# Performance work log

Hardware: AMD Instinct MI355X
Metric: run time of the kernel (lower is better)

The kernel has to match this reference:

```python
import jax, jax.numpy as jnp
import numpy as np

# irreps '64x0e+32x1o+16x2e' as (mul, ir_dim, is_scalar)
IRREPS = [(64, 1, True), (32, 3, False), (16, 5, False)]
DIM = sum(m * d for m, d, _ in IRREPS)          # 240
NUM_FEATURES = sum(m for m, _, _ in IRREPS)      # 112
NUM_SCALAR = sum(m for m, _, s in IRREPS if s)   # 64
NUM_TYPE = 10
EPS = 1e-5
BATCH = 200000


def setup_inputs() -> dict:
    key = jax.random.key(0)
    k1, k2 = jax.random.split(key)
    x = jax.random.normal(k1, (BATCH, DIM), dtype=jnp.float32)
    input_type = jax.random.randint(k2, (BATCH,), 0, NUM_TYPE)
    weight = jnp.ones((NUM_TYPE, NUM_FEATURES), dtype=jnp.float32)
    bias = jnp.zeros((NUM_TYPE, NUM_SCALAR), dtype=jnp.float32)
    return {"x": x, "input_type": input_type, "weight": weight, "bias": bias}


def _type_mean(vals, input_type, counts):
    # scatter_mean over the batch dim into NUM_TYPE slots
    s = jax.ops.segment_sum(vals, input_type, num_segments=NUM_TYPE)
    return s / counts[:, None]


def reference(x, input_type, weight, bias):
    batch, dim = x.shape
    xr = x.reshape(batch, 1, dim)  # middle dim (no extra ... dims here)
    counts = jnp.maximum(
        jax.ops.segment_sum(jnp.ones((batch,), x.dtype), input_type, num_segments=NUM_TYPE),
        1.0,
    )
    fields = []
    ix = iw = ib = 0
    for mul, d, is_scalar in IRREPS:
        field = xr[:, :, ix:ix + mul * d].reshape(batch, -1, mul, d)
        ix += mul * d
        if is_scalar:
            fm = field.mean(1).reshape(batch, mul)                 # (batch, mul)
            fm = _type_mean(fm, input_type, counts)                # (num_type, mul)
            field = field - fm[input_type][:, None, :, None]
        # normalization='component': mean over ir dim; reduce='mean' over middle dim
        fn = jnp.square(field).mean(3).mean(1)                     # (batch, mul)
        fn = _type_mean(fn, input_type, counts)                    # (num_type, mul)
        fn = jax.lax.rsqrt(fn + EPS)
        fn = fn * weight[:, iw:iw + mul]
        iw += mul
        field = field * fn[input_type][:, None, :, None]
        if is_scalar:
            field = field + bias[:, ib:ib + mul][input_type][:, None, :, None]
            ib += mul
        fields.append(field.reshape(batch, -1, mul * d))
    out = jnp.concatenate(fields, axis=2)
    return out.reshape(batch, dim)
```

## Files before the change

### kernel.cpp

```cpp
#include <hip/hip_runtime.h>

#define DIM 240
#define NTYPE 10
#define NFEAT 112
#define NSLOT 176
#define NRED  1770
#define PSTRIDE 1792
#define RCHUNK 32
#define EPSV 1e-5f


__global__ __launch_bounds__(256) void stats_kernel(const float* __restrict__ x,
        const int* __restrict__ type, float* __restrict__ partial, int B, int nblk)
{
    const int tid = threadIdx.x;
    const bool active = tid < DIM;
    const bool isScalar = tid < 64;

    float accA[NTYPE], accB[NTYPE];
#pragma unroll
    for (int t = 0; t < NTYPE; t++) { accA[t] = 0.f; accB[t] = 0.f; }

    const float inactAdd = (tid == 255) ? 1.f : 0.f;

    auto accum = [&](int ty, float v) {
        const float v2 = v * v;
        const float addA = active ? (isScalar ? v : v2) : inactAdd;
#pragma unroll
        for (int t = 0; t < NTYPE; t++) {
            if (t == ty) { accA[t] += addA; accB[t] += v2; }
        }
    };

    const int stride = nblk * 8;
    for (int row0 = blockIdx.x * 8; row0 + 7 < B; row0 += stride) {
        int ty[8];
#pragma unroll
        for (int j = 0; j < 8; j++) ty[j] = type[row0 + j];
        float v[8];
#pragma unroll
        for (int j = 0; j < 8; j++) v[j] = 0.f;
        if (active) {
            const float* p = x + (size_t)row0 * DIM + tid;
#pragma unroll
            for (int j = 0; j < 8; j++) v[j] = p[j * DIM];
        }
#pragma unroll
        for (int j = 0; j < 8; j++) accum(ty[j], v[j]);
    }
    if (blockIdx.x == 0) {
        for (int r = B & ~7; r < B; r++) {
            const int ty0 = type[r];
            float v = active ? x[(size_t)r * DIM + tid] : 0.f;
            accum(ty0, v);
        }
    }

    __shared__ float sAcc[NRED];
    for (int i = tid; i < NRED; i += 256) sAcc[i] = 0.f;
    __syncthreads();

    if (isScalar) {
#pragma unroll
        for (int t = 0; t < NTYPE; t++) {
            sAcc[t * NSLOT + tid] = accA[t];
            sAcc[t * NSLOT + 64 + tid] = accB[t];
        }
    } else if (tid < 160) {
        const int ch = (tid - 64) / 3;
#pragma unroll
        for (int t = 0; t < NTYPE; t++)
            atomicAdd(&sAcc[t * NSLOT + 128 + ch], accA[t]);
    } else if (tid < DIM) {
        const int ch = (tid - 160) / 5;
#pragma unroll
        for (int t = 0; t < NTYPE; t++)
            atomicAdd(&sAcc[t * NSLOT + 160 + ch], accA[t]);
    } else if (tid == 255) {
#pragma unroll
        for (int t = 0; t < NTYPE; t++)
            sAcc[NTYPE * NSLOT + t] = accA[t];
    }
    __syncthreads();

    float* __restrict__ dst = partial + (size_t)blockIdx.x * PSTRIDE;
    for (int i = tid; i < NRED; i += 256) dst[i] = sAcc[i];
}

__global__ __launch_bounds__(256) void reduce1_kernel(const float* __restrict__ partial,
        float* __restrict__ gpart, int nblk)
{
    const int colChunk = blockIdx.x % 7;
    const int rowChunk = blockIdx.x / 7;
    const int col = colChunk * 256 + threadIdx.x;
    const int r0 = (rowChunk * nblk) / RCHUNK;
    const int r1 = ((rowChunk + 1) * nblk) / RCHUNK;
    float acc = 0.f;
#pragma unroll 8
    for (int r = r0; r < r1; r++)
        acc += partial[(size_t)r * PSTRIDE + col];
    gpart[rowChunk * PSTRIDE + col] = acc;
}

__global__ __launch_bounds__(256) void finalize_kernel(const float* __restrict__ gpart,
        const float* __restrict__ weight, const float* __restrict__ bias,
        float* __restrict__ params)
{
    const int t = blockIdx.x;
    const int c = threadIdx.x;

    __shared__ float scnt;
    if (c == 0) {
        float cs = 0.f;
#pragma unroll
        for (int k = 0; k < RCHUNK; k++)
            cs += gpart[k * PSTRIDE + NTYPE * NSLOT + t];
        scnt = fmaxf(cs, 1.f);
    }
    __syncthreads();
    if (c >= DIM) return;
    const float inv = 1.f / scnt;

    float sub = 0.f, mul, bia = 0.f;
    if (c < 64) {
        float S = 0.f, Q = 0.f;
#pragma unroll
        for (int k = 0; k < RCHUNK; k++) {
            const float* p = gpart + k * PSTRIDE + t * NSLOT;
            S += p[c]; Q += p[64 + c];
        }
        const float mean = S * inv;
        float var = Q * inv - mean * mean;
        var = fmaxf(var, 0.f);
        mul = rsqrtf(var + EPSV) * weight[t * NFEAT + c];
        sub = mean;
        bia = bias[t * 64 + c];
    } else if (c < 160) {
        const int ch = (c - 64) / 3;
        float N = 0.f;
#pragma unroll
        for (int k = 0; k < RCHUNK; k++)
            N += gpart[k * PSTRIDE + t * NSLOT + 128 + ch];
        mul = rsqrtf(N * inv * (1.f / 3.f) + EPSV) * weight[t * NFEAT + 64 + ch];
    } else {
        const int ch = (c - 160) / 5;
        float N = 0.f;
#pragma unroll
        for (int k = 0; k < RCHUNK; k++)
            N += gpart[k * PSTRIDE + t * NSLOT + 160 + ch];
        mul = rsqrtf(N * inv * 0.2f + EPSV) * weight[t * NFEAT + 96 + ch];
    }
    float* p = params + t * 720;
    p[c] = sub;
    p[240 + c] = mul;
    p[480 + c] = bia;
}

__global__ __launch_bounds__(256) void apply_kernel(const float* __restrict__ x,
        const int* __restrict__ type, const float* __restrict__ params,
        float* __restrict__ out, int B, int nblocks)
{
    __shared__ float4 sp[NTYPE * 180];
    const int tid = threadIdx.x;
    const float4* __restrict__ pg = (const float4*)params;
    for (int i = tid; i < NTYPE * 180; i += 256) sp[i] = pg[i];
    __syncthreads();

    const int rBase = tid / 60;
    const int c4 = tid - rBase * 60;
    const bool active = tid < 240;
    const float4* __restrict__ xv = (const float4*)x;
    float4* __restrict__ ov = (float4*)out;

    const int rstride = nblocks * 8;
    for (int row0 = blockIdx.x * 8; row0 < B; row0 += rstride) {
        const int r0 = row0 + rBase;
        const int r1 = r0 + 4;
        const bool a0 = active && r0 < B;
        const bool a1 = active && r1 < B;
        int t0 = 0, t1 = 0;
        float4 v0 = {0, 0, 0, 0}, v1 = {0, 0, 0, 0};
        if (a0) { t0 = type[r0]; v0 = xv[(size_t)r0 * 60 + c4]; }
        if (a1) { t1 = type[r1]; v1 = xv[(size_t)r1 * 60 + c4]; }
        if (a0) {
            const float4 s = sp[t0 * 180 + c4];
            const float4 m = sp[t0 * 180 + 60 + c4];
            const float4 b = sp[t0 * 180 + 120 + c4];
            float4 o;
            o.x = (v0.x - s.x) * m.x + b.x;
            o.y = (v0.y - s.y) * m.y + b.y;
            o.z = (v0.z - s.z) * m.z + b.z;
            o.w = (v0.w - s.w) * m.w + b.w;
            ov[(size_t)r0 * 60 + c4] = o;
        }
        if (a1) {
            const float4 s = sp[t1 * 180 + c4];
            const float4 m = sp[t1 * 180 + 60 + c4];
            const float4 b = sp[t1 * 180 + 120 + c4];
            float4 o;
            o.x = (v1.x - s.x) * m.x + b.x;
            o.y = (v1.y - s.y) * m.y + b.y;
            o.z = (v1.z - s.z) * m.z + b.z;
            o.w = (v1.w - s.w) * m.w + b.w;
            ov[(size_t)r1 * 60 + c4] = o;
        }
    }
}

extern "C" void kernel_launch(void* const* d_in, const int* in_sizes, int n_in,
                              void* d_out, int out_size, void* d_ws, size_t ws_size,
                              hipStream_t stream) {
    const float* x      = (const float*)d_in[0];
    const int*   type   = (const int*)d_in[1];
    const float* weight = (const float*)d_in[2];
    const float* bias   = (const float*)d_in[3];
    float* out = (float*)d_out;
    float* ws  = (float*)d_ws;
    const int B = in_sizes[0] / DIM;

    int nblk = 2048;
    size_t fixed = (size_t)RCHUNK * PSTRIDE + 7200;
    size_t need_floats = (size_t)nblk * PSTRIDE + fixed;
    if (ws_size < need_floats * 4) {
        nblk = (int)((ws_size / 4 - fixed) / PSTRIDE);
        if (nblk < 1) nblk = 1;
    }
    float* partial = ws;
    float* gpart   = ws + (size_t)nblk * PSTRIDE;
    float* params  = gpart + (size_t)RCHUNK * PSTRIDE;

    hipLaunchKernelGGL(stats_kernel, dim3(nblk), dim3(256), 0, stream,
                       x, type, partial, B, nblk);
    hipLaunchKernelGGL(reduce1_kernel, dim3(7 * RCHUNK), dim3(256), 0, stream,
                       partial, gpart, nblk);
    hipLaunchKernelGGL(finalize_kernel, dim3(NTYPE), dim3(256), 0, stream,
                       gpart, weight, bias, params);
    hipLaunchKernelGGL(apply_kernel, dim3(1280), dim3(256), 0, stream,
                       x, type, params, out, B, 1280);
}
```

Measured before the change: 398.8 us.

## Flatten apply kernel indexing, add nontemporal stores, deepen stats row batching

The apply kernel now walks the output as a flat array of float4 elements using a grid-stride loop with four loads in flight per thread. Row indices come from a multiply-shift divide by 60, so all 256 threads stay active instead of 240. Output writes use nontemporal stores to avoid polluting cache. The stats kernel processes 16 rows per iteration instead of 8 for more memory parallelism, and the apply grid grows to 2048 blocks; the larger unroll raises register pressure.

Result: faster. 379.9 us (-4.7%).

```diff
diff --git a/kernel.cpp b/kernel.cpp
--- a/kernel.cpp
+++ b/kernel.cpp
@@ -7,7 +7,10 @@
 #define NRED  1770
 #define PSTRIDE 1792
 #define RCHUNK 32
+#define SROWS 16
 #define EPSV 1e-5f
+
+typedef float nf4 __attribute__((ext_vector_type(4)));
 
 
 __global__ __launch_bounds__(256) void stats_kernel(const float* __restrict__ x,
@@ -32,24 +35,24 @@
         }
     };
 
-    const int stride = nblk * 8;
-    for (int row0 = blockIdx.x * 8; row0 + 7 < B; row0 += stride) {
-        int ty[8];
-#pragma unroll
-        for (int j = 0; j < 8; j++) ty[j] = type[row0 + j];
-        float v[8];
-#pragma unroll
-        for (int j = 0; j < 8; j++) v[j] = 0.f;
+    const int stride = nblk * SROWS;
+    for (int row0 = blockIdx.x * SROWS; row0 + (SROWS - 1) < B; row0 += stride) {
+        int ty[SROWS];
+#pragma unroll
+        for (int j = 0; j < SROWS; j++) ty[j] = type[row0 + j];
+        float v[SROWS];
+#pragma unroll
+        for (int j = 0; j < SROWS; j++) v[j] = 0.f;
         if (active) {
             const float* p = x + (size_t)row0 * DIM + tid;
 #pragma unroll
-            for (int j = 0; j < 8; j++) v[j] = p[j * DIM];
-        }
-#pragma unroll
-        for (int j = 0; j < 8; j++) accum(ty[j], v[j]);
+            for (int j = 0; j < SROWS; j++) v[j] = p[j * DIM];
+        }
+#pragma unroll
+        for (int j = 0; j < SROWS; j++) accum(ty[j], v[j]);
     }
     if (blockIdx.x == 0) {
-        for (int r = B & ~7; r < B; r++) {
+        for (int r = B & ~(SROWS - 1); r < B; r++) {
             const int ty0 = type[r];
             float v = active ? x[(size_t)r * DIM + tid] : 0.f;
             accum(ty0, v);
@@ -160,49 +163,54 @@
         const int* __restrict__ type, const float* __restrict__ params,
         float* __restrict__ out, int B, int nblocks)
 {
-    __shared__ float4 sp[NTYPE * 180];
+    __shared__ nf4 sp[NTYPE * 180];
     const int tid = threadIdx.x;
-    const float4* __restrict__ pg = (const float4*)params;
+    const nf4* __restrict__ pg = (const nf4*)params;
     for (int i = tid; i < NTYPE * 180; i += 256) sp[i] = pg[i];
     __syncthreads();
 
-    const int rBase = tid / 60;
-    const int c4 = tid - rBase * 60;
-    const bool active = tid < 240;
-    const float4* __restrict__ xv = (const float4*)x;
-    float4* __restrict__ ov = (float4*)out;
-
-    const int rstride = nblocks * 8;
-    for (int row0 = blockIdx.x * 8; row0 < B; row0 += rstride) {
-        const int r0 = row0 + rBase;
-        const int r1 = r0 + 4;
-        const bool a0 = active && r0 < B;
-        const bool a1 = active && r1 < B;
-        int t0 = 0, t1 = 0;
-        float4 v0 = {0, 0, 0, 0}, v1 = {0, 0, 0, 0};
-        if (a0) { t0 = type[r0]; v0 = xv[(size_t)r0 * 60 + c4]; }
-        if (a1) { t1 = type[r1]; v1 = xv[(size_t)r1 * 60 + c4]; }
+    const int total = B * 60;
+    const nf4* __restrict__ xv = (const nf4*)x;
+    nf4* __restrict__ ov = (nf4*)out;
+    const int estride = nblocks * 256;
+
+    for (int base = blockIdx.x * 256 + tid; base < total; base += estride * 4) {
+        int e0 = base, e1 = base + estride, e2 = base + 2 * estride, e3 = base + 3 * estride;
+        const bool a0 = e0 < total, a1 = e1 < total, a2 = e2 < total, a3 = e3 < total;
+        const int r0 = (int)(((unsigned long long)(unsigned)e0 * 2290649225ull) >> 37);
+        const int r1 = a1 ? (int)(((unsigned long long)(unsigned)e1 * 2290649225ull) >> 37) : 0;
+        const int r2 = a2 ? (int)(((unsigned long long)(unsigned)e2 * 2290649225ull) >> 37) : 0;
+        const int r3 = a3 ? (int)(((unsigned long long)(unsigned)e3 * 2290649225ull) >> 37) : 0;
+        const int c0 = e0 - r0 * 60, c1 = e1 - r1 * 60, c2 = e2 - r2 * 60, c3 = e3 - r3 * 60;
+        int t0 = 0, t1 = 0, t2 = 0, t3 = 0;
+        nf4 v0 = {0,0,0,0}, v1 = {0,0,0,0}, v2 = {0,0,0,0}, v3 = {0,0,0,0};
+        if (a0) { t0 = type[r0]; v0 = xv[e0]; }
+        if (a1) { t1 = type[r1]; v1 = xv[e1]; }
+        if (a2) { t2 = type[r2]; v2 = xv[e2]; }
+        if (a3) { t3 = type[r3]; v3 = xv[e3]; }
         if (a0) {
-            const float4 s = sp[t0 * 180 + c4];
-            const float4 m = sp[t0 * 180 + 60 + c4];
-            const float4 b = sp[t0 * 180 + 120 + c4];
-            float4 o;
-            o.x = (v0.x - s.x) * m.x + b.x;
-            o.y = (v0.y - s.y) * m.y + b.y;
-            o.z = (v0.z - s.z) * m.z + b.z;
-            o.w = (v0.w - s.w) * m.w + b.w;
-            ov[(size_t)r0 * 60 + c4] = o;
+            const nf4 s = sp[t0 * 180 + c0];
+            const nf4 m = sp[t0 * 180 + 60 + c0];
+            const nf4 b = sp[t0 * 180 + 120 + c0];
+            __builtin_nontemporal_store((v0 - s) * m + b, &ov[e0]);
         }
         if (a1) {
-            const float4 s = sp[t1 * 180 + c4];
-            const float4 m = sp[t1 * 180 + 60 + c4];
-            const float4 b = sp[t1 * 180 + 120 + c4];
-            float4 o;
-            o.x = (v1.x - s.x) * m.x + b.x;
-            o.y = (v1.y - s.y) * m.y + b.y;
-            o.z = (v1.z - s.z) * m.z + b.z;
-            o.w = (v1.w - s.w) * m.w + b.w;
-            ov[(size_t)r1 * 60 + c4] = o;
+            const nf4 s = sp[t1 * 180 + c1];
+            const nf4 m = sp[t1 * 180 + 60 + c1];
+            const nf4 b = sp[t1 * 180 + 120 + c1];
+            __builtin_nontemporal_store((v1 - s) * m + b, &ov[e1]);
+        }
+        if (a2) {
+            const nf4 s = sp[t2 * 180 + c2];
+            const nf4 m = sp[t2 * 180 + 60 + c2];
+            const nf4 b = sp[t2 * 180 + 120 + c2];
+            __builtin_nontemporal_store((v2 - s) * m + b, &ov[e2]);
+        }
+        if (a3) {
+            const nf4 s = sp[t3 * 180 + c3];
+            const nf4 m = sp[t3 * 180 + 60 + c3];
+            const nf4 b = sp[t3 * 180 + 120 + c3];
+            __builtin_nontemporal_store((v3 - s) * m + b, &ov[e3]);
         }
     }
 }
@@ -235,6 +243,6 @@
                        partial, gpart, nblk);
     hipLaunchKernelGGL(finalize_kernel, dim3(NTYPE), dim3(256), 0, stream,
                        gpart, weight, bias, params);
-    hipLaunchKernelGGL(apply_kernel, dim3(1280), dim3(256), 0, stream,
-                       x, type, params, out, B, 1280);
-}
+    hipLaunchKernelGGL(apply_kernel, dim3(2048), dim3(256), 0, stream,
+                       x, type, params, out, B, 2048);
+}
```
